# Performance work log

Measured on AMD Instinct MI355X. Metric: run time of the kernel, lower is better.

The kernel has to match this reference:

```python
import jax, jax.numpy as jnp
import numpy as np

ROWS, COLS = 1024, 1024
N_NODES = ROWS * COLS
RHO_W = 1000.0      # water density
RHO_I = 917.0       # ice density (unused in output path, kept for fidelity)
GRAV = 9.81
SEC_PER_A = 31556926.0
FLOW_COEFF = 0.0405
FLOW_EXP = 1.25     # 5/4
N_ITERS = 32        # fixed-point iterations for MFD flow accumulation


def _raster_links(rows, cols):
    ids = np.arange(rows * cols, dtype=np.int32).reshape(rows, cols)
    src_h = ids[:, :-1].ravel(); dst_h = ids[:, 1:].ravel()
    src_v = ids[:-1, :].ravel(); dst_v = ids[1:, :].ravel()
    return (np.concatenate([src_h, src_v]), np.concatenate([dst_h, dst_v]))


def setup_inputs() -> dict:
    key = jax.random.key(0)
    k1, k2, k3, k4 = jax.random.split(key, 4)
    melt_rate = jax.random.uniform(k1, (N_NODES,), jnp.float32) * 10.0          # m/a
    bedrock_elevation = jax.random.normal(k2, (N_NODES,), jnp.float32) * 500.0  # m
    water_pressure = jax.random.uniform(k3, (N_NODES,), jnp.float32) * 1.0e6    # Pa
    cell_area = jnp.full((N_NODES,), 1.0e4, jnp.float32)                        # 100m cells
    conduit_size = jax.random.uniform(k4, (N_NODES,), jnp.float32) + 0.01
    # landlab-style status: 0 = core node, 1 = fixed-value boundary (perimeter)
    status = np.zeros((ROWS, COLS), dtype=np.int32)
    status[0, :] = 1; status[-1, :] = 1; status[:, 0] = 1; status[:, -1] = 1
    src, dst = _raster_links(ROWS, COLS)
    return {
        "melt_rate": melt_rate,
        "bedrock_elevation": bedrock_elevation,
        "water_pressure": water_pressure,
        "cell_area": cell_area,
        "conduit_size": conduit_size,
        "status_at_node": jnp.asarray(status.ravel()),
        "link_src": jnp.asarray(src),
        "link_dst": jnp.asarray(dst),
    }


def reference(melt_rate, bedrock_elevation, water_pressure, cell_area,
              conduit_size, status_at_node, link_src, link_dst):
    n = melt_rate.shape[0]
    seg = lambda d, i: jax.ops.segment_sum(d, i, num_segments=n)

    # hydraulic potential (surface FlowDirectorMFD routes on)
    phi = RHO_W * GRAV * bedrock_elevation + water_pressure
    # local runoff input at each node
    runoff = melt_rate * cell_area / SEC_PER_A

    # MFD: split each node's outflow among downslope neighbors, proportional
    # to the positive potential drop along each link (unit link length).
    core = (status_at_node == 0)
    dphi = phi[link_src] - phi[link_dst]
    drop_fwd = jnp.maximum(dphi, 0.0) * core[link_src]   # src -> dst
    drop_bwd = jnp.maximum(-dphi, 0.0) * core[link_dst]  # dst -> src
    total_drop = seg(drop_fwd, link_src) + seg(drop_bwd, link_dst)
    s_safe = jnp.where(total_drop > 0.0, total_drop, 1.0)
    frac_fwd = drop_fwd / s_safe[link_src]
    frac_bwd = drop_bwd / s_safe[link_dst]

    # flow accumulation on the drainage DAG: Q = runoff + P^T Q (fixed-point)
    def step(q, _):
        inflow = seg(frac_fwd * q[link_src], link_dst) + seg(frac_bwd * q[link_dst], link_src)
        return runoff + inflow, None

    discharge, _ = jax.lax.scan(step, runoff, None, length=N_ITERS)

    # calc_hydraulic_gradient, masked to core nodes (status == 0)
    gradient = (discharge * FLOW_COEFF * conduit_size ** FLOW_EXP) ** 2
    return jnp.where(status_at_node == 0, gradient, 0.0)
```

## Files before the change

### kernel.cpp

```cpp
#include <hip/hip_runtime.h>

#define ROWS 1024
#define COLS 1024
#define NN (ROWS*COLS)

#define TILE_H 32
#define TILE_W 64
#define HALO   8
#define RH     48
#define RW     80
#define RC     (RH*RW)
#define SPR    (RW/4)
#define NSTRIP (RC/4)
#define NT     320
#define SPT    3

static constexpr float RHOG    = 1000.0f * 9.81f;
static constexpr float INV_SEC = 1.0f / 31556926.0f;
static constexpr float FLOWC   = 0.0405f;

__global__ __launch_bounds__(256) void k_pre(
        const float* __restrict__ bed, const float* __restrict__ pw,
        const int* __restrict__ status,
        const float* __restrict__ melt, const float* __restrict__ area,
        float* __restrict__ phi, float* __restrict__ inv,
        float* __restrict__ runoff) {
    int i = blockIdx.x * 256 + threadIdx.x;
    int r = i >> 10, c = i & (COLS - 1);
    float p = RHOG * bed[i] + pw[i];
    float t = 0.0f;
    if (c > 0)        t += fmaxf(p - (RHOG * bed[i - 1]    + pw[i - 1]),    0.0f);
    if (c < COLS - 1) t += fmaxf(p - (RHOG * bed[i + 1]    + pw[i + 1]),    0.0f);
    if (r > 0)        t += fmaxf(p - (RHOG * bed[i - COLS] + pw[i - COLS]), 0.0f);
    if (r < ROWS - 1) t += fmaxf(p - (RHOG * bed[i + COLS] + pw[i + COLS]), 0.0f);
    phi[i]    = p;
    inv[i]    = (status[i] == 0 && t > 0.0f) ? (1.0f / t) : 0.0f;
    runoff[i] = melt[i] * area[i] * INV_SEC;
}

__device__ __forceinline__ float4 gld4(const float* __restrict__ p, int g, bool in) {
    if (in) return *reinterpret_cast<const float4*>(p + g);
    return make_float4(0.f, 0.f, 0.f, 0.f);
}

template <bool FIRST, bool FINAL>
__global__ __launch_bounds__(NT) void k_fused(
        const float* __restrict__ phi_g, const float* __restrict__ inv_g,
        const float* __restrict__ runoff_g, const float* __restrict__ qin,
        float* __restrict__ qout,
        const float* __restrict__ cond, const int* __restrict__ status) {
    __shared__ float lds[2][RC];
    const int tid = threadIdx.x;
    const int r0 = (int)blockIdx.y * TILE_H - HALO;
    const int c0 = (int)blockIdx.x * TILE_W - HALO;

    int xC[SPT], xW[SPT], xE[SPT], xN[SPT], xS[SPT], gg[SPT];
    int srA[SPT], scA[SPT];
    bool inA[SPT];
    float4 ro[SPT], q0[SPT];
    int4 dd[SPT];

#pragma unroll
    for (int j = 0; j < SPT; ++j) {
        int sid = tid + j * NT;
        int sr = sid / SPR, sc = sid - sr * SPR;
        srA[j] = sr; scA[j] = sc;
        int iC = sr * RW + 4 * sc;
        xC[j] = iC;
        xW[j] = (sc > 0)       ? iC - 1  : iC;
        xE[j] = (sc < SPR - 1) ? iC + 4  : iC;
        xN[j] = (sr > 0)       ? iC - RW : iC;
        xS[j] = (sr < RH - 1)  ? iC + RW : iC;
        int gr = r0 + sr, gc = c0 + 4 * sc;
        bool in = (gr >= 0) & (gr < ROWS) & (gc >= 0) & (gc < COLS);
        inA[j] = in;
        gg[j] = gr * COLS + gc;
        int drow = min(sr, RH - 1 - sr);
        int cc = 4 * sc;
        dd[j].x = min(drow, min(cc,     RW - 1 - cc));
        dd[j].y = min(drow, min(cc + 1, RW - 2 - cc));
        dd[j].z = min(drow, min(cc + 2, RW - 3 - cc));
        dd[j].w = min(drow, min(cc + 3, RW - 4 - cc));
    }

    float4 pcA[SPT], icA[SPT];
#pragma unroll
    for (int j = 0; j < SPT; ++j) {
        float4 p4 = gld4(phi_g, gg[j], inA[j]);
        float4 i4 = gld4(inv_g, gg[j], inA[j]);
        ro[j] = gld4(runoff_g, gg[j], inA[j]);
        if (!FIRST) q0[j] = gld4(qin, gg[j], inA[j]);
        else        q0[j] = ro[j];
        pcA[j] = p4; icA[j] = i4;
        *reinterpret_cast<float4*>(&lds[0][xC[j]]) = p4;
        *reinterpret_cast<float4*>(&lds[1][xC[j]]) = i4;
    }
    __syncthreads();

    float4 w0[SPT], w1[SPT], w2[SPT], w3[SPT];
#pragma unroll
    for (int j = 0; j < SPT; ++j) {
        float4 pc = pcA[j], ic = icA[j];
        float pw_ = lds[0][xW[j]], pe_ = lds[0][xE[j]];
        float iw_ = lds[1][xW[j]], ie_ = lds[1][xE[j]];
        float4 pn = *reinterpret_cast<const float4*>(&lds[0][xN[j]]);
        float4 ps = *reinterpret_cast<const float4*>(&lds[0][xS[j]]);
        float4 vn = *reinterpret_cast<const float4*>(&lds[1][xN[j]]);
        float4 vs = *reinterpret_cast<const float4*>(&lds[1][xS[j]]);
        w0[j].x = fmaxf(pw_  - pc.x, 0.f) * iw_;
        w0[j].y = fmaxf(pc.x - pc.y, 0.f) * ic.x;
        w0[j].z = fmaxf(pc.y - pc.z, 0.f) * ic.y;
        w0[j].w = fmaxf(pc.z - pc.w, 0.f) * ic.z;
        w1[j].x = fmaxf(pc.y - pc.x, 0.f) * ic.y;
        w1[j].y = fmaxf(pc.z - pc.y, 0.f) * ic.z;
        w1[j].z = fmaxf(pc.w - pc.z, 0.f) * ic.w;
        w1[j].w = fmaxf(pe_  - pc.w, 0.f) * ie_;
        w2[j].x = fmaxf(pn.x - pc.x, 0.f) * vn.x;
        w2[j].y = fmaxf(pn.y - pc.y, 0.f) * vn.y;
        w2[j].z = fmaxf(pn.z - pc.z, 0.f) * vn.z;
        w2[j].w = fmaxf(pn.w - pc.w, 0.f) * vn.w;
        w3[j].x = fmaxf(ps.x - pc.x, 0.f) * vs.x;
        w3[j].y = fmaxf(ps.y - pc.y, 0.f) * vs.y;
        w3[j].z = fmaxf(ps.z - pc.z, 0.f) * vs.z;
        w3[j].w = fmaxf(ps.w - pc.w, 0.f) * vs.w;
    }
    __syncthreads();

#pragma unroll
    for (int j = 0; j < SPT; ++j)
        *reinterpret_cast<float4*>(&lds[0][xC[j]]) = q0[j];
    __syncthreads();

    for (int s = 0; s < HALO; ++s) {
        const float* __restrict__ src = lds[s & 1];
        float* __restrict__ dst = lds[(s + 1) & 1];
#pragma unroll
        for (int j = 0; j < SPT; ++j) {
            float4 cv = *reinterpret_cast<const float4*>(&src[xC[j]]);
            float wv = src[xW[j]], ev = src[xE[j]];
            float4 nv = *reinterpret_cast<const float4*>(&src[xN[j]]);
            float4 sv = *reinterpret_cast<const float4*>(&src[xS[j]]);
            float4 acc;
            acc.x = fmaf(w0[j].x, wv,   ro[j].x);
            acc.y = fmaf(w0[j].y, cv.x, ro[j].y);
            acc.z = fmaf(w0[j].z, cv.y, ro[j].z);
            acc.w = fmaf(w0[j].w, cv.z, ro[j].w);
            acc.x = fmaf(w1[j].x, cv.y, acc.x);
            acc.y = fmaf(w1[j].y, cv.z, acc.y);
            acc.z = fmaf(w1[j].z, cv.w, acc.z);
            acc.w = fmaf(w1[j].w, ev,   acc.w);
            acc.x = fmaf(w2[j].x, nv.x, acc.x);
            acc.y = fmaf(w2[j].y, nv.y, acc.y);
            acc.z = fmaf(w2[j].z, nv.z, acc.z);
            acc.w = fmaf(w2[j].w, nv.w, acc.w);
            acc.x = fmaf(w3[j].x, sv.x, acc.x);
            acc.y = fmaf(w3[j].y, sv.y, acc.y);
            acc.z = fmaf(w3[j].z, sv.z, acc.z);
            acc.w = fmaf(w3[j].w, sv.w, acc.w);
            float4 out;
            out.x = (s < dd[j].x) ? acc.x : cv.x;
            out.y = (s < dd[j].y) ? acc.y : cv.y;
            out.z = (s < dd[j].z) ? acc.z : cv.z;
            out.w = (s < dd[j].w) ? acc.w : cv.w;
            *reinterpret_cast<float4*>(&dst[xC[j]]) = out;
        }
        __syncthreads();
    }

#pragma unroll
    for (int j = 0; j < SPT; ++j) {
        int sr = srA[j], sc = scA[j];
        if (sr >= HALO && sr < RH - HALO && sc >= HALO / 4 && sc < SPR - HALO / 4) {
            float4 q = *reinterpret_cast<const float4*>(&lds[0][xC[j]]);
            int g = gg[j];
            if (FINAL) {
                float4 c4 = *reinterpret_cast<const float4*>(cond + g);
                int4 st   = *reinterpret_cast<const int4*>(status + g);
                float4 o;
                float t;
                t = q.x * FLOWC * (c4.x * sqrtf(sqrtf(c4.x))); o.x = (st.x == 0) ? t * t : 0.f;
                t = q.y * FLOWC * (c4.y * sqrtf(sqrtf(c4.y))); o.y = (st.y == 0) ? t * t : 0.f;
                t = q.z * FLOWC * (c4.z * sqrtf(sqrtf(c4.z))); o.z = (st.z == 0) ? t * t : 0.f;
                t = q.w * FLOWC * (c4.w * sqrtf(sqrtf(c4.w))); o.w = (st.w == 0) ? t * t : 0.f;
                *reinterpret_cast<float4*>(qout + g) = o;
            } else {
                *reinterpret_cast<float4*>(qout + g) = q;
            }
        }
    }
}

extern "C" void kernel_launch(void* const* d_in, const int* in_sizes, int n_in,
                              void* d_out, int out_size, void* d_ws, size_t ws_size,
                              hipStream_t stream) {
    const float* melt   = (const float*)d_in[0];
    const float* bed    = (const float*)d_in[1];
    const float* pw     = (const float*)d_in[2];
    const float* area   = (const float*)d_in[3];
    const float* cond   = (const float*)d_in[4];
    const int*   status = (const int*)d_in[5];
    float* out = (float*)d_out;

    char* ws = (char*)d_ws;
    float* phi    = (float*)(ws);
    float* inv    = (float*)(ws + 4ull  * NN);
    float* runoff = (float*)(ws + 8ull  * NN);
    float* qA     = (float*)(ws + 12ull * NN);
    float* qB     = (float*)(ws + 16ull * NN);

    k_pre<<<dim3(NN / 256), dim3(256), 0, stream>>>(bed, pw, status, melt, area,
                                                    phi, inv, runoff);

    dim3 grid(COLS / TILE_W, ROWS / TILE_H), block(NT);
    k_fused<true,  false><<<grid, block, 0, stream>>>(phi, inv, runoff, runoff, qA, nullptr, nullptr);
    k_fused<false, false><<<grid, block, 0, stream>>>(phi, inv, runoff, qA, qB, nullptr, nullptr);
    k_fused<false, false><<<grid, block, 0, stream>>>(phi, inv, runoff, qB, qA, nullptr, nullptr);
    k_fused<false, true ><<<grid, block, 0, stream>>>(phi, inv, runoff, qA, out, cond, status);
}
```

Measured before the change: 155.8 us.

## Precompute per-node link weights once and keep own strip in registers

```diff
diff --git a/kernel.cpp b/kernel.cpp
--- a/kernel.cpp
+++ b/kernel.cpp
@@ -19,61 +19,98 @@
 static constexpr float INV_SEC = 1.0f / 31556926.0f;
 static constexpr float FLOWC   = 0.0405f;
 
-__global__ __launch_bounds__(256) void k_pre(
+__device__ __forceinline__ float4 gld4(const float* __restrict__ p, int g, bool in) {
+    if (in) return *reinterpret_cast<const float4*>(p + g);
+    return make_float4(0.f, 0.f, 0.f, 0.f);
+}
+
+__global__ __launch_bounds__(256) void k_phi_inv(
         const float* __restrict__ bed, const float* __restrict__ pw,
         const int* __restrict__ status,
-        const float* __restrict__ melt, const float* __restrict__ area,
-        float* __restrict__ phi, float* __restrict__ inv,
-        float* __restrict__ runoff) {
+        float* __restrict__ phi, float* __restrict__ inv) {
     int i = blockIdx.x * 256 + threadIdx.x;
     int r = i >> 10, c = i & (COLS - 1);
     float p = RHOG * bed[i] + pw[i];
-    float t = 0.0f;
-    if (c > 0)        t += fmaxf(p - (RHOG * bed[i - 1]    + pw[i - 1]),    0.0f);
-    if (c < COLS - 1) t += fmaxf(p - (RHOG * bed[i + 1]    + pw[i + 1]),    0.0f);
-    if (r > 0)        t += fmaxf(p - (RHOG * bed[i - COLS] + pw[i - COLS]), 0.0f);
-    if (r < ROWS - 1) t += fmaxf(p - (RHOG * bed[i + COLS] + pw[i + COLS]), 0.0f);
-    phi[i]    = p;
-    inv[i]    = (status[i] == 0 && t > 0.0f) ? (1.0f / t) : 0.0f;
-    runoff[i] = melt[i] * area[i] * INV_SEC;
-}
-
-__device__ __forceinline__ float4 gld4(const float* __restrict__ p, int g, bool in) {
-    if (in) return *reinterpret_cast<const float4*>(p + g);
-    return make_float4(0.f, 0.f, 0.f, 0.f);
+    float t = 0.f;
+    if (c > 0)        t += fmaxf(p - (RHOG * bed[i - 1]    + pw[i - 1]),    0.f);
+    if (c < COLS - 1) t += fmaxf(p - (RHOG * bed[i + 1]    + pw[i + 1]),    0.f);
+    if (r > 0)        t += fmaxf(p - (RHOG * bed[i - COLS] + pw[i - COLS]), 0.f);
+    if (r < ROWS - 1) t += fmaxf(p - (RHOG * bed[i + COLS] + pw[i + COLS]), 0.f);
+    phi[i] = p;
+    inv[i] = (status[i] == 0 && t > 0.f) ? (1.f / t) : 0.f;
+}
+
+__global__ __launch_bounds__(256) void k_wgt(
+        const float* __restrict__ phi, const float* __restrict__ inv,
+        const float* __restrict__ melt, const float* __restrict__ area,
+        float4* __restrict__ w, float* __restrict__ runoff) {
+    int t = blockIdx.x * 256 + threadIdx.x;
+    int i = t * 4;
+    int r = i >> 10, c = i & (COLS - 1);
+    float4 pc = *reinterpret_cast<const float4*>(phi + i);
+    float4 ic = *reinterpret_cast<const float4*>(inv + i);
+    bool hn = (r > 0), hs = (r < ROWS - 1);
+    float4 z = make_float4(0.f, 0.f, 0.f, 0.f);
+    float4 pn = hn ? *reinterpret_cast<const float4*>(phi + i - COLS) : z;
+    float4 vn = hn ? *reinterpret_cast<const float4*>(inv + i - COLS) : z;
+    float4 ps = hs ? *reinterpret_cast<const float4*>(phi + i + COLS) : z;
+    float4 vs = hs ? *reinterpret_cast<const float4*>(inv + i + COLS) : z;
+    float pw_ = (c > 0) ? phi[i - 1] : 0.f, iw_ = (c > 0) ? inv[i - 1] : 0.f;
+    float pe_ = (c < COLS - 4) ? phi[i + 4] : 0.f, ie_ = (c < COLS - 4) ? inv[i + 4] : 0.f;
+    w[i + 0] = make_float4(fmaxf(pw_  - pc.x, 0.f) * iw_,
+                           fmaxf(pc.y - pc.x, 0.f) * ic.y,
+                           fmaxf(pn.x - pc.x, 0.f) * vn.x,
+                           fmaxf(ps.x - pc.x, 0.f) * vs.x);
+    w[i + 1] = make_float4(fmaxf(pc.x - pc.y, 0.f) * ic.x,
+                           fmaxf(pc.z - pc.y, 0.f) * ic.z,
+                           fmaxf(pn.y - pc.y, 0.f) * vn.y,
+                           fmaxf(ps.y - pc.y, 0.f) * vs.y);
+    w[i + 2] = make_float4(fmaxf(pc.y - pc.z, 0.f) * ic.y,
+                           fmaxf(pc.w - pc.z, 0.f) * ic.w,
+                           fmaxf(pn.z - pc.z, 0.f) * vn.z,
+                           fmaxf(ps.z - pc.z, 0.f) * vs.z);
+    w[i + 3] = make_float4(fmaxf(pc.z - pc.w, 0.f) * ic.z,
+                           fmaxf(pe_  - pc.w, 0.f) * ie_,
+                           fmaxf(pn.w - pc.w, 0.f) * vn.w,
+                           fmaxf(ps.w - pc.w, 0.f) * vs.w);
+    float4 m4 = *reinterpret_cast<const float4*>(melt + i);
+    float4 a4 = *reinterpret_cast<const float4*>(area + i);
+    *reinterpret_cast<float4*>(runoff + i) =
+        make_float4(m4.x * a4.x * INV_SEC, m4.y * a4.y * INV_SEC,
+                    m4.z * a4.z * INV_SEC, m4.w * a4.w * INV_SEC);
 }
 
 template <bool FIRST, bool FINAL>
 __global__ __launch_bounds__(NT) void k_fused(
-        const float* __restrict__ phi_g, const float* __restrict__ inv_g,
-        const float* __restrict__ runoff_g, const float* __restrict__ qin,
-        float* __restrict__ qout,
+        const float4* __restrict__ w_g, const float* __restrict__ run_g,
+        const float* __restrict__ qin, float* __restrict__ qout,
         const float* __restrict__ cond, const int* __restrict__ status) {
-    __shared__ float lds[2][RC];
+    __shared__ float ldsq[2][RC];
+    __shared__ float plane[2][2][NSTRIP];
     const int tid = threadIdx.x;
     const int r0 = (int)blockIdx.y * TILE_H - HALO;
     const int c0 = (int)blockIdx.x * TILE_W - HALO;
 
-    int xC[SPT], xW[SPT], xE[SPT], xN[SPT], xS[SPT], gg[SPT];
-    int srA[SPT], scA[SPT];
-    bool inA[SPT];
-    float4 ro[SPT], q0[SPT];
+    int xC[SPT], xN[SPT], xS[SPT], gg[SPT], sidA[SPT], sidW[SPT], sidE[SPT];
+    bool inA[SPT], inter[SPT];
+    float4 ro[SPT], oq[SPT];
+    float4 wc0[SPT], wc1[SPT], wc2[SPT], wc3[SPT];
     int4 dd[SPT];
 
 #pragma unroll
     for (int j = 0; j < SPT; ++j) {
         int sid = tid + j * NT;
+        sidA[j] = sid;
+        sidW[j] = (sid > 0) ? sid - 1 : 0;
+        sidE[j] = (sid < NSTRIP - 1) ? sid + 1 : NSTRIP - 1;
         int sr = sid / SPR, sc = sid - sr * SPR;
-        srA[j] = sr; scA[j] = sc;
         int iC = sr * RW + 4 * sc;
         xC[j] = iC;
-        xW[j] = (sc > 0)       ? iC - 1  : iC;
-        xE[j] = (sc < SPR - 1) ? iC + 4  : iC;
-        xN[j] = (sr > 0)       ? iC - RW : iC;
-        xS[j] = (sr < RH - 1)  ? iC + RW : iC;
+        xN[j] = (sr > 0)      ? iC - RW : iC;
+        xS[j] = (sr < RH - 1) ? iC + RW : iC;
         int gr = r0 + sr, gc = c0 + 4 * sc;
-        bool in = (gr >= 0) & (gr < ROWS) & (gc >= 0) & (gc < COLS);
-        inA[j] = in;
+        inA[j] = (gr >= 0) & (gr < ROWS) & (gc >= 0) & (gc < COLS);
+        inter[j] = (sr >= HALO) & (sr < RH - HALO) & (sc >= HALO / 4) & (sc < SPR - HALO / 4);
         gg[j] = gr * COLS + gc;
         int drow = min(sr, RH - 1 - sr);
         int cc = 4 * sc;
@@ -83,96 +120,72 @@
         dd[j].w = min(drow, min(cc + 3, RW - 4 - cc));
     }
 
-    float4 pcA[SPT], icA[SPT];
 #pragma unroll
     for (int j = 0; j < SPT; ++j) {
-        float4 p4 = gld4(phi_g, gg[j], inA[j]);
-        float4 i4 = gld4(inv_g, gg[j], inA[j]);
-        ro[j] = gld4(runoff_g, gg[j], inA[j]);
-        if (!FIRST) q0[j] = gld4(qin, gg[j], inA[j]);
-        else        q0[j] = ro[j];
-        pcA[j] = p4; icA[j] = i4;
-        *reinterpret_cast<float4*>(&lds[0][xC[j]]) = p4;
-        *reinterpret_cast<float4*>(&lds[1][xC[j]]) = i4;
+        const float* wb = (const float*)(w_g + gg[j]);
+        bool in = inA[j];
+        wc0[j] = gld4(wb, 0,  in);
+        wc1[j] = gld4(wb, 4,  in);
+        wc2[j] = gld4(wb, 8,  in);
+        wc3[j] = gld4(wb, 12, in);
+        ro[j]  = gld4(run_g, gg[j], in);
+        float4 q0 = FIRST ? ro[j] : gld4(qin, gg[j], in);
+        oq[j] = q0;
+        *reinterpret_cast<float4*>(&ldsq[0][xC[j]]) = q0;
+        plane[0][0][sidA[j]] = q0.x;
+        plane[0][1][sidA[j]] = q0.w;
     }
     __syncthreads();
 
-    float4 w0[SPT], w1[SPT], w2[SPT], w3[SPT];
-#pragma unroll
-    for (int j = 0; j < SPT; ++j) {
-        float4 pc = pcA[j], ic = icA[j];
-        float pw_ = lds[0][xW[j]], pe_ = lds[0][xE[j]];
-        float iw_ = lds[1][xW[j]], ie_ = lds[1][xE[j]];
-        float4 pn = *reinterpret_cast<const float4*>(&lds[0][xN[j]]);
-        float4 ps = *reinterpret_cast<const float4*>(&lds[0][xS[j]]);
-        float4 vn = *reinterpret_cast<const float4*>(&lds[1][xN[j]]);
-        float4 vs = *reinterpret_cast<const float4*>(&lds[1][xS[j]]);
-        w0[j].x = fmaxf(pw_  - pc.x, 0.f) * iw_;
-        w0[j].y = fmaxf(pc.x - pc.y, 0.f) * ic.x;
-        w0[j].z = fmaxf(pc.y - pc.z, 0.f) * ic.y;
-        w0[j].w = fmaxf(pc.z - pc.w, 0.f) * ic.z;
-        w1[j].x = fmaxf(pc.y - pc.x, 0.f) * ic.y;
-        w1[j].y = fmaxf(pc.z - pc.y, 0.f) * ic.z;
-        w1[j].z = fmaxf(pc.w - pc.z, 0.f) * ic.w;
-        w1[j].w = fmaxf(pe_  - pc.w, 0.f) * ie_;
-        w2[j].x = fmaxf(pn.x - pc.x, 0.f) * vn.x;
-        w2[j].y = fmaxf(pn.y - pc.y, 0.f) * vn.y;
-        w2[j].z = fmaxf(pn.z - pc.z, 0.f) * vn.z;
-        w2[j].w = fmaxf(pn.w - pc.w, 0.f) * vn.w;
-        w3[j].x = fmaxf(ps.x - pc.x, 0.f) * vs.x;
-        w3[j].y = fmaxf(ps.y - pc.y, 0.f) * vs.y;
-        w3[j].z = fmaxf(ps.z - pc.z, 0.f) * vs.z;
-        w3[j].w = fmaxf(ps.w - pc.w, 0.f) * vs.w;
-    }
-    __syncthreads();
-
-#pragma unroll
-    for (int j = 0; j < SPT; ++j)
-        *reinterpret_cast<float4*>(&lds[0][xC[j]]) = q0[j];
-    __syncthreads();
-
     for (int s = 0; s < HALO; ++s) {
-        const float* __restrict__ src = lds[s & 1];
-        float* __restrict__ dst = lds[(s + 1) & 1];
+        const float* __restrict__ src = ldsq[s & 1];
+        float* __restrict__ dst = ldsq[(s + 1) & 1];
+        const float* __restrict__ pL = plane[s & 1][0];
+        const float* __restrict__ pR = plane[s & 1][1];
+        float* __restrict__ qL = plane[(s + 1) & 1][0];
+        float* __restrict__ qR = plane[(s + 1) & 1][1];
 #pragma unroll
         for (int j = 0; j < SPT; ++j) {
-            float4 cv = *reinterpret_cast<const float4*>(&src[xC[j]]);
-            float wv = src[xW[j]], ev = src[xE[j]];
+            float4 cv = oq[j];
+            float wv = pR[sidW[j]];
+            float ev = pL[sidE[j]];
             float4 nv = *reinterpret_cast<const float4*>(&src[xN[j]]);
             float4 sv = *reinterpret_cast<const float4*>(&src[xS[j]]);
             float4 acc;
-            acc.x = fmaf(w0[j].x, wv,   ro[j].x);
-            acc.y = fmaf(w0[j].y, cv.x, ro[j].y);
-            acc.z = fmaf(w0[j].z, cv.y, ro[j].z);
-            acc.w = fmaf(w0[j].w, cv.z, ro[j].w);
-            acc.x = fmaf(w1[j].x, cv.y, acc.x);
-            acc.y = fmaf(w1[j].y, cv.z, acc.y);
-            acc.z = fmaf(w1[j].z, cv.w, acc.z);
-            acc.w = fmaf(w1[j].w, ev,   acc.w);
-            acc.x = fmaf(w2[j].x, nv.x, acc.x);
-            acc.y = fmaf(w2[j].y, nv.y, acc.y);
-            acc.z = fmaf(w2[j].z, nv.z, acc.z);
-            acc.w = fmaf(w2[j].w, nv.w, acc.w);
-            acc.x = fmaf(w3[j].x, sv.x, acc.x);
-            acc.y = fmaf(w3[j].y, sv.y, acc.y);
-            acc.z = fmaf(w3[j].z, sv.z, acc.z);
-            acc.w = fmaf(w3[j].w, sv.w, acc.w);
-            float4 out;
-            out.x = (s < dd[j].x) ? acc.x : cv.x;
-            out.y = (s < dd[j].y) ? acc.y : cv.y;
-            out.z = (s < dd[j].z) ? acc.z : cv.z;
-            out.w = (s < dd[j].w) ? acc.w : cv.w;
-            *reinterpret_cast<float4*>(&dst[xC[j]]) = out;
+            acc.x = fmaf(wc0[j].x, wv,   ro[j].x);
+            acc.y = fmaf(wc1[j].x, cv.x, ro[j].y);
+            acc.z = fmaf(wc2[j].x, cv.y, ro[j].z);
+            acc.w = fmaf(wc3[j].x, cv.z, ro[j].w);
+            acc.x = fmaf(wc0[j].y, cv.y, acc.x);
+            acc.y = fmaf(wc1[j].y, cv.z, acc.y);
+            acc.z = fmaf(wc2[j].y, cv.w, acc.z);
+            acc.w = fmaf(wc3[j].y, ev,   acc.w);
+            acc.x = fmaf(wc0[j].z, nv.x, acc.x);
+            acc.y = fmaf(wc1[j].z, nv.y, acc.y);
+            acc.z = fmaf(wc2[j].z, nv.z, acc.z);
+            acc.w = fmaf(wc3[j].z, nv.w, acc.w);
+            acc.x = fmaf(wc0[j].w, sv.x, acc.x);
+            acc.y = fmaf(wc1[j].w, sv.y, acc.y);
+            acc.z = fmaf(wc2[j].w, sv.z, acc.z);
+            acc.w = fmaf(wc3[j].w, sv.w, acc.w);
+            float4 o;
+            o.x = (s < dd[j].x) ? acc.x : cv.x;
+            o.y = (s < dd[j].y) ? acc.y : cv.y;
+            o.z = (s < dd[j].z) ? acc.z : cv.z;
+            o.w = (s < dd[j].w) ? acc.w : cv.w;
+            oq[j] = o;
+            *reinterpret_cast<float4*>(&dst[xC[j]]) = o;
+            qL[sidA[j]] = o.x;
+            qR[sidA[j]] = o.w;
         }
         __syncthreads();
     }
 
 #pragma unroll
     for (int j = 0; j < SPT; ++j) {
-        int sr = srA[j], sc = scA[j];
-        if (sr >= HALO && sr < RH - HALO && sc >= HALO / 4 && sc < SPR - HALO / 4) {
-            float4 q = *reinterpret_cast<const float4*>(&lds[0][xC[j]]);
+        if (inter[j]) {
             int g = gg[j];
+            float4 q = oq[j];
             if (FINAL) {
                 float4 c4 = *reinterpret_cast<const float4*>(cond + g);
                 int4 st   = *reinterpret_cast<const int4*>(status + g);
@@ -202,18 +215,19 @@
     float* out = (float*)d_out;
 
     char* ws = (char*)d_ws;
-    float* phi    = (float*)(ws);
-    float* inv    = (float*)(ws + 4ull  * NN);
-    float* runoff = (float*)(ws + 8ull  * NN);
-    float* qA     = (float*)(ws + 12ull * NN);
-    float* qB     = (float*)(ws + 16ull * NN);
-
-    k_pre<<<dim3(NN / 256), dim3(256), 0, stream>>>(bed, pw, status, melt, area,
-                                                    phi, inv, runoff);
+    float*  phi    = (float*)(ws);
+    float*  inv    = (float*)(ws + 4ull  * NN);
+    float4* w      = (float4*)(ws + 8ull  * NN);
+    float*  runoff = (float*)(ws + 24ull * NN);
+    float*  qA     = (float*)(ws + 28ull * NN);
+    float*  qB     = (float*)(ws + 32ull * NN);
+
+    k_phi_inv<<<dim3(NN / 256), dim3(256), 0, stream>>>(bed, pw, status, phi, inv);
+    k_wgt<<<dim3(NN / 1024), dim3(256), 0, stream>>>(phi, inv, melt, area, w, runoff);
 
     dim3 grid(COLS / TILE_W, ROWS / TILE_H), block(NT);
-    k_fused<true,  false><<<grid, block, 0, stream>>>(phi, inv, runoff, runoff, qA, nullptr, nullptr);
-    k_fused<false, false><<<grid, block, 0, stream>>>(phi, inv, runoff, qA, qB, nullptr, nullptr);
-    k_fused<false, false><<<grid, block, 0, stream>>>(phi, inv, runoff, qB, qA, nullptr, nullptr);
-    k_fused<false, true ><<<grid, block, 0, stream>>>(phi, inv, runoff, qA, out, cond, status);
-}
+    k_fused<true,  false><<<grid, block, 0, stream>>>(w, runoff, runoff, qA, nullptr, nullptr);
+    k_fused<false, false><<<grid, block, 0, stream>>>(w, runoff, qA, qB, nullptr, nullptr);
+    k_fused<false, false><<<grid, block, 0, stream>>>(w, runoff, qB, qA, nullptr, nullptr);
+    k_fused<false, true ><<<grid, block, 0, stream>>>(w, runoff, qA, out, cond, status);
+}
```

After: 172.4 us. +10.6%, slower.
